# Kernel tuning notes

Measured on AMD Instinct MI355X. Metric: run time of the kernel, lower is better.

Reference implementation:

```python
import jax, jax.numpy as jnp
import numpy as np

B, T, D_IN, D_STATE, N_NEURONS, D_OUT = 256, 512, 128, 128, 2048, 64


def setup_inputs() -> dict:
    key = jax.random.key(0)
    ks = jax.random.split(key, 6)
    d_aug = D_IN + D_STATE
    seq = jax.random.normal(ks[0], (B, T, D_IN), dtype=jnp.float32)
    # hypersphere-style encoders: unit-norm rows over the augmented input space
    enc = jax.random.normal(ks[1], (N_NEURONS, d_aug), dtype=jnp.float32)
    encoders = enc / jnp.linalg.norm(enc, axis=1, keepdims=True)
    gain = jax.random.uniform(ks[2], (N_NEURONS,), minval=0.5, maxval=2.0, dtype=jnp.float32)
    bias = jax.random.normal(ks[3], (N_NEURONS,), dtype=jnp.float32)
    # decoders are analytically fit in the original; use small random values so the
    # recurrent feedback path carries nontrivial signal
    state_decoders = jax.random.normal(ks[4], (N_NEURONS, D_STATE), dtype=jnp.float32) * 0.02
    decoders = jax.random.normal(ks[5], (N_NEURONS, D_OUT), dtype=jnp.float32) * 0.02
    return {"seq": seq, "encoders": encoders, "gain": gain, "bias": bias,
            "state_decoders": state_decoders, "decoders": decoders}


def reference(seq, encoders, gain, bias, state_decoders, decoders):
    # seq: (B, T, d_in); encoders: (N, d_in+d_state); state_decoders: (N, d_state)
    b = seq.shape[0]
    d_state = state_decoders.shape[1]
    n = encoders.shape[0]
    seq_t = jnp.swapaxes(seq, 0, 1)  # (T, B, d_in)

    def step(carry, u):
        s, _ = carry  # s: (B, d_state)
        x_aug = jnp.concatenate([u, s], axis=-1)          # (B, d_in+d_state)
        a = jax.nn.relu(gain * (x_aug @ encoders.T) + bias)  # (B, N)
        return (a @ state_decoders, a), None

    init = (jnp.zeros((b, d_state), seq.dtype), jnp.zeros((b, n), seq.dtype))
    (_, a_final), _ = jax.lax.scan(step, init, seq_t)
    return a_final @ decoders  # (B, d_out)
```

## Files before the change

kernel.cpp:

```cpp
#include <hip/hip_runtime.h>


constexpr int CB   = 256;
constexpr int CT   = 512;
constexpr int DIN  = 128;
constexpr int DST  = 128;
constexpr int DOUT = 64;
constexpr int DAUG = 256;

constexpr int NBG = 8;
constexpr int NNG = 16;
constexpr int BT  = 32;
constexpr int NT  = 128;

constexpr int EPAD = 264;
constexpr int APAD = 136;

using f32x4  = __attribute__((ext_vector_type(4))) float;
using bf16x8 = __attribute__((ext_vector_type(8))) short;

__device__ __forceinline__ short f2b(float x) {
  unsigned u = __builtin_bit_cast(unsigned, x);
  u += 0x7fffu + ((u >> 16) & 1u);
  return (short)(u >> 16);
}
__device__ __forceinline__ short4 f2b4(float4 v) {
  return make_short4(f2b(v.x), f2b(v.y), f2b(v.z), f2b(v.w));
}

__global__ void nef_init(float* Sbuf, unsigned int* ctrs, float* out) {
  int idx = blockIdx.x * blockDim.x + threadIdx.x;
  int stride = gridDim.x * blockDim.x;
  for (int i = idx; i < 4 * CB * DST; i += stride) Sbuf[i] = 0.f;
  for (int i = idx; i < CB * DOUT; i += stride) out[i] = 0.f;
  if (idx < 16 * 64) ctrs[idx] = 0u;
}

__global__ void __launch_bounds__(256) nef_main(
    const float* __restrict__ seq,  const float* __restrict__ enc,
    const float* __restrict__ gainp,const float* __restrict__ biasp,
    const float* __restrict__ sdec, const float* __restrict__ dec,
    float* __restrict__ out, float* __restrict__ Sbuf, unsigned int* ctrs)
{
  __shared__ short E_lds[NT][EPAD];
  __shared__ short SDT_lds[DST][APAD];
  __shared__ short X_lds[BT][EPAD];
  __shared__ short A_lds[BT][APAD];
  __shared__ float gain_lds[NT];
  __shared__ float bias_lds[NT];

  const int tid  = threadIdx.x;
  const int bg   = blockIdx.x & 7;
  const int ng   = blockIdx.x >> 3;
  const int b0   = bg * BT;
  const int n0   = ng * NT;
  const int wave = tid >> 6;
  const int lane = tid & 63;
  const int l15  = lane & 15;
  const int lhi  = lane >> 4;
  const int kbase = lhi * 8;

  for (int i = 0; i < 32; ++i) {
    int fidx = i * 256 + tid;
    int row = fidx >> 6, c4 = fidx & 63;
    const float4 v = *(const float4*)(enc + (size_t)(n0 + row) * DAUG + (c4 << 2));
    *(short4*)&E_lds[row][c4 << 2] = f2b4(v);
  }
  for (int i = 0; i < 16; ++i) {
    int fidx = i * 256 + tid;
    int n = fidx >> 5, c4 = fidx & 31;
    const float4 v = *(const float4*)(sdec + (size_t)(n0 + n) * DST + (c4 << 2));
    SDT_lds[(c4 << 2) + 0][n] = f2b(v.x);
    SDT_lds[(c4 << 2) + 1][n] = f2b(v.y);
    SDT_lds[(c4 << 2) + 2][n] = f2b(v.z);
    SDT_lds[(c4 << 2) + 3][n] = f2b(v.w);
  }
  if (tid < NT) { gain_lds[tid] = gainp[n0 + tid]; bias_lds[tid] = biasp[n0 + tid]; }

  unsigned int* ctr = ctrs + bg * 64;
  const int nsub0 = wave * 32, nsub1 = nsub0 + 16;

  float4 pu[4];
#pragma unroll
  for (int i = 0; i < 4; ++i) {
    int fidx = i * 256 + tid;
    int row = fidx >> 5, c4 = fidx & 31;
    pu[i] = *(const float4*)(seq + ((size_t)(b0 + row) * CT + 0) * DIN + (c4 << 2));
  }

  for (int t = 0; t < CT; ++t) {
    {
      float* Sz = Sbuf + ((t + 2) & 3) * (CB * DST);
      __hip_atomic_store(&Sz[b0 * DST + ng * 256 + tid], 0.f,
                         __ATOMIC_RELAXED, __HIP_MEMORY_SCOPE_AGENT);
    }
#pragma unroll
    for (int i = 0; i < 4; ++i) {
      int fidx = i * 256 + tid;
      int row = fidx >> 5, c4 = fidx & 31;
      *(short4*)&X_lds[row][c4 << 2] = f2b4(pu[i]);
    }
    if (t + 1 < CT) {
#pragma unroll
      for (int i = 0; i < 4; ++i) {
        int fidx = i * 256 + tid;
        int row = fidx >> 5, c4 = fidx & 31;
        pu[i] = *(const float4*)(seq + ((size_t)(b0 + row) * CT + (t + 1)) * DIN + (c4 << 2));
      }
    }
    if (t > 0) {
      unsigned int tgt = 16u * (unsigned)t, guard = 0;
      while (__hip_atomic_load(ctr, __ATOMIC_RELAXED, __HIP_MEMORY_SCOPE_AGENT) < tgt) {
        __builtin_amdgcn_s_sleep(1);
        if (++guard > 100000u) break;
      }
    }
    {
      const float* Sr = Sbuf + (t & 3) * (CB * DST);
#pragma unroll
      for (int i = 0; i < 2; ++i) {
        int idx8 = i * 256 + tid;
        int row = idx8 >> 4, c8 = idx8 & 15;
        const unsigned long long* p =
            (const unsigned long long*)(Sr + (size_t)(b0 + row) * DST + c8 * 8);
        short s8[8];
#pragma unroll
        for (int q = 0; q < 4; ++q) {
          unsigned long long w = __hip_atomic_load(p + q, __ATOMIC_RELAXED,
                                                   __HIP_MEMORY_SCOPE_AGENT);
          s8[2 * q]     = f2b(__builtin_bit_cast(float, (unsigned)(w & 0xffffffffu)));
          s8[2 * q + 1] = f2b(__builtin_bit_cast(float, (unsigned)(w >> 32)));
        }
        *(short4*)&X_lds[row][DIN + c8 * 8]     = make_short4(s8[0], s8[1], s8[2], s8[3]);
        *(short4*)&X_lds[row][DIN + c8 * 8 + 4] = make_short4(s8[4], s8[5], s8[6], s8[7]);
      }
    }
    __syncthreads();

    f32x4 acc00 = {0,0,0,0}, acc01 = {0,0,0,0}, acc10 = {0,0,0,0}, acc11 = {0,0,0,0};
#pragma unroll
    for (int kk = 0; kk < 8; ++kk) {
      bf16x8 a0 = *(const bf16x8*)&X_lds[l15][kk * 32 + kbase];
      bf16x8 a1 = *(const bf16x8*)&X_lds[16 + l15][kk * 32 + kbase];
      bf16x8 e0 = *(const bf16x8*)&E_lds[nsub0 + l15][kk * 32 + kbase];
      bf16x8 e1 = *(const bf16x8*)&E_lds[nsub1 + l15][kk * 32 + kbase];
      acc00 = __builtin_amdgcn_mfma_f32_16x16x32_bf16(a0, e0, acc00, 0, 0, 0);
      acc01 = __builtin_amdgcn_mfma_f32_16x16x32_bf16(a0, e1, acc01, 0, 0, 0);
      acc10 = __builtin_amdgcn_mfma_f32_16x16x32_bf16(a1, e0, acc10, 0, 0, 0);
      acc11 = __builtin_amdgcn_mfma_f32_16x16x32_bf16(a1, e1, acc11, 0, 0, 0);
    }
    {
      const int nc0 = nsub0 + l15, nc1 = nsub1 + l15;
      const float g0 = gain_lds[nc0], bi0 = bias_lds[nc0];
      const float g1 = gain_lds[nc1], bi1 = bias_lds[nc1];
#pragma unroll
      for (int j = 0; j < 4; ++j) {
        A_lds[lhi * 4 + j][nc0]      = f2b(fmaxf(g0 * acc00[j] + bi0, 0.f));
        A_lds[lhi * 4 + j][nc1]      = f2b(fmaxf(g1 * acc01[j] + bi1, 0.f));
        A_lds[16 + lhi * 4 + j][nc0] = f2b(fmaxf(g0 * acc10[j] + bi0, 0.f));
        A_lds[16 + lhi * 4 + j][nc1] = f2b(fmaxf(g1 * acc11[j] + bi1, 0.f));
      }
    }
    __syncthreads();

    if (t != CT - 1) {
      f32x4 p00 = {0,0,0,0}, p01 = {0,0,0,0}, p10 = {0,0,0,0}, p11 = {0,0,0,0};
      const int d0 = nsub0 + l15, d1 = nsub1 + l15;
#pragma unroll
      for (int kk = 0; kk < 4; ++kk) {
        bf16x8 a0 = *(const bf16x8*)&A_lds[l15][kk * 32 + kbase];
        bf16x8 a1 = *(const bf16x8*)&A_lds[16 + l15][kk * 32 + kbase];
        bf16x8 s0 = *(const bf16x8*)&SDT_lds[d0][kk * 32 + kbase];
        bf16x8 s1 = *(const bf16x8*)&SDT_lds[d1][kk * 32 + kbase];
        p00 = __builtin_amdgcn_mfma_f32_16x16x32_bf16(a0, s0, p00, 0, 0, 0);
        p01 = __builtin_amdgcn_mfma_f32_16x16x32_bf16(a0, s1, p01, 0, 0, 0);
        p10 = __builtin_amdgcn_mfma_f32_16x16x32_bf16(a1, s0, p10, 0, 0, 0);
        p11 = __builtin_amdgcn_mfma_f32_16x16x32_bf16(a1, s1, p11, 0, 0, 0);
      }
      float* Sw = Sbuf + ((t + 1) & 3) * (CB * DST);
#pragma unroll
      for (int j = 0; j < 4; ++j) {
        unsafeAtomicAdd(&Sw[(size_t)(b0 + lhi * 4 + j) * DST + d0],      p00[j]);
        unsafeAtomicAdd(&Sw[(size_t)(b0 + lhi * 4 + j) * DST + d1],      p01[j]);
        unsafeAtomicAdd(&Sw[(size_t)(b0 + 16 + lhi * 4 + j) * DST + d0], p10[j]);
        unsafeAtomicAdd(&Sw[(size_t)(b0 + 16 + lhi * 4 + j) * DST + d1], p11[j]);
      }
      __syncthreads();
      if (tid == 0) atomicAdd(ctr, 1u);
    } else {
      f32x4 o0 = {0,0,0,0}, o1 = {0,0,0,0};
      const int ocol = wave * 16 + l15;
#pragma unroll
      for (int kk = 0; kk < 4; ++kk) {
        bf16x8 a0 = *(const bf16x8*)&A_lds[l15][kk * 32 + kbase];
        bf16x8 a1 = *(const bf16x8*)&A_lds[16 + l15][kk * 32 + kbase];
        bf16x8 bfD;
#pragma unroll
        for (int j = 0; j < 8; ++j)
          bfD[j] = f2b(dec[(size_t)(n0 + kk * 32 + kbase + j) * DOUT + ocol]);
        o0 = __builtin_amdgcn_mfma_f32_16x16x32_bf16(a0, bfD, o0, 0, 0, 0);
        o1 = __builtin_amdgcn_mfma_f32_16x16x32_bf16(a1, bfD, o1, 0, 0, 0);
      }
#pragma unroll
      for (int j = 0; j < 4; ++j) {
        unsafeAtomicAdd(&out[(size_t)(b0 + lhi * 4 + j) * DOUT + ocol], o0[j]);
        unsafeAtomicAdd(&out[(size_t)(b0 + 16 + lhi * 4 + j) * DOUT + ocol], o1[j]);
      }
    }
  }
}

extern "C" void kernel_launch(void* const* d_in, const int* in_sizes, int n_in,
                              void* d_out, int out_size, void* d_ws, size_t ws_size,
                              hipStream_t stream) {
  const float* seq   = (const float*)d_in[0];
  const float* enc   = (const float*)d_in[1];
  const float* gainp = (const float*)d_in[2];
  const float* biasp = (const float*)d_in[3];
  const float* sdec  = (const float*)d_in[4];
  const float* dec   = (const float*)d_in[5];
  float* out = (float*)d_out;

  float* Sbuf = (float*)d_ws;
  unsigned int* ctrs = (unsigned int*)((char*)d_ws + (size_t)4 * CB * DST * sizeof(float));

  nef_init<<<128, 256, 0, stream>>>(Sbuf, ctrs, out);
  nef_main<<<dim3(NBG * NNG), dim3(256), 0, stream>>>(seq, enc, gainp, biasp,
                                                      sdec, dec, out, Sbuf, ctrs);
}
```

Baseline: 1.673 ms.

## Overlap input half of encoder GEMM with state wait, use packed fp16 atomics

The encoder matmul is split so the input-driven half (first 128 K columns) is computed before waiting on the cross-block state counter, hiding part of the recurrence latency. The shared state buffer becomes packed fp16 pairs, updated with global_atomic_pk_add_f16 after a lane shuffle, which halves atomic count and traffic. Each wave now signals the counter itself after s_waitcnt instead of a block barrier plus a single thread. Next-step input staging moves to the end of the step. Accumulating the state in fp16 reduces precision in the recurrent path and adds a risk of overflow or rounding error.

```diff
diff --git a/kernel.cpp b/kernel.cpp
--- a/kernel.cpp
+++ b/kernel.cpp
@@ -27,11 +27,23 @@
 __device__ __forceinline__ short4 f2b4(float4 v) {
   return make_short4(f2b(v.x), f2b(v.y), f2b(v.z), f2b(v.w));
 }
-
-__global__ void nef_init(float* Sbuf, unsigned int* ctrs, float* out) {
+__device__ __forceinline__ float h2f(unsigned short h) {
+  return (float)__builtin_bit_cast(_Float16, h);
+}
+__device__ __forceinline__ unsigned pack_h2(float lo, float hi) {
+  unsigned short l = __builtin_bit_cast(unsigned short, (_Float16)lo);
+  unsigned short h = __builtin_bit_cast(unsigned short, (_Float16)hi);
+  return (unsigned)l | ((unsigned)h << 16);
+}
+__device__ __forceinline__ void pk_add_f16(unsigned* addr, unsigned val) {
+  asm volatile("global_atomic_pk_add_f16 %0, %1, off"
+               :: "v"((unsigned long long)addr), "v"(val) : "memory");
+}
+
+__global__ void nef_init(unsigned* Sbuf, unsigned int* ctrs, float* out) {
   int idx = blockIdx.x * blockDim.x + threadIdx.x;
   int stride = gridDim.x * blockDim.x;
-  for (int i = idx; i < 4 * CB * DST; i += stride) Sbuf[i] = 0.f;
+  for (int i = idx; i < 4 * CB * 64; i += stride) Sbuf[i] = 0u;
   for (int i = idx; i < CB * DOUT; i += stride) out[i] = 0.f;
   if (idx < 16 * 64) ctrs[idx] = 0u;
 }
@@ -40,7 +52,7 @@
     const float* __restrict__ seq,  const float* __restrict__ enc,
     const float* __restrict__ gainp,const float* __restrict__ biasp,
     const float* __restrict__ sdec, const float* __restrict__ dec,
-    float* __restrict__ out, float* __restrict__ Sbuf, unsigned int* ctrs)
+    float* __restrict__ out, unsigned* __restrict__ Sbuf, unsigned int* ctrs)
 {
   __shared__ short E_lds[NT][EPAD];
   __shared__ short SDT_lds[DST][APAD];
@@ -87,59 +99,63 @@
     int row = fidx >> 5, c4 = fidx & 31;
     pu[i] = *(const float4*)(seq + ((size_t)(b0 + row) * CT + 0) * DIN + (c4 << 2));
   }
+#pragma unroll
+  for (int i = 0; i < 4; ++i) {
+    int fidx = i * 256 + tid;
+    int row = fidx >> 5, c4 = fidx & 31;
+    *(short4*)&X_lds[row][c4 << 2] = f2b4(pu[i]);
+    pu[i] = *(const float4*)(seq + ((size_t)(b0 + row) * CT + 1) * DIN + (c4 << 2));
+  }
+  __syncthreads();
 
   for (int t = 0; t < CT; ++t) {
-    {
-      float* Sz = Sbuf + ((t + 2) & 3) * (CB * DST);
-      __hip_atomic_store(&Sz[b0 * DST + ng * 256 + tid], 0.f,
+    if (tid < 128) {
+      unsigned* Sz = Sbuf + ((t + 2) & 3) * (CB * 64);
+      __hip_atomic_store(&Sz[b0 * 64 + ng * 128 + tid], 0u,
                          __ATOMIC_RELAXED, __HIP_MEMORY_SCOPE_AGENT);
     }
-#pragma unroll
-    for (int i = 0; i < 4; ++i) {
-      int fidx = i * 256 + tid;
-      int row = fidx >> 5, c4 = fidx & 31;
-      *(short4*)&X_lds[row][c4 << 2] = f2b4(pu[i]);
-    }
-    if (t + 1 < CT) {
-#pragma unroll
-      for (int i = 0; i < 4; ++i) {
-        int fidx = i * 256 + tid;
-        int row = fidx >> 5, c4 = fidx & 31;
-        pu[i] = *(const float4*)(seq + ((size_t)(b0 + row) * CT + (t + 1)) * DIN + (c4 << 2));
-      }
-    }
+
+    f32x4 acc00 = {0,0,0,0}, acc01 = {0,0,0,0}, acc10 = {0,0,0,0}, acc11 = {0,0,0,0};
+#pragma unroll
+    for (int kk = 0; kk < 4; ++kk) {
+      bf16x8 a0 = *(const bf16x8*)&X_lds[l15][kk * 32 + kbase];
+      bf16x8 a1 = *(const bf16x8*)&X_lds[16 + l15][kk * 32 + kbase];
+      bf16x8 e0 = *(const bf16x8*)&E_lds[nsub0 + l15][kk * 32 + kbase];
+      bf16x8 e1 = *(const bf16x8*)&E_lds[nsub1 + l15][kk * 32 + kbase];
+      acc00 = __builtin_amdgcn_mfma_f32_16x16x32_bf16(a0, e0, acc00, 0, 0, 0);
+      acc01 = __builtin_amdgcn_mfma_f32_16x16x32_bf16(a0, e1, acc01, 0, 0, 0);
+      acc10 = __builtin_amdgcn_mfma_f32_16x16x32_bf16(a1, e0, acc10, 0, 0, 0);
+      acc11 = __builtin_amdgcn_mfma_f32_16x16x32_bf16(a1, e1, acc11, 0, 0, 0);
+    }
+
     if (t > 0) {
-      unsigned int tgt = 16u * (unsigned)t, guard = 0;
+      unsigned int tgt = 64u * (unsigned)t, guard = 0;
       while (__hip_atomic_load(ctr, __ATOMIC_RELAXED, __HIP_MEMORY_SCOPE_AGENT) < tgt) {
         __builtin_amdgcn_s_sleep(1);
         if (++guard > 100000u) break;
       }
     }
     {
-      const float* Sr = Sbuf + (t & 3) * (CB * DST);
-#pragma unroll
-      for (int i = 0; i < 2; ++i) {
-        int idx8 = i * 256 + tid;
-        int row = idx8 >> 4, c8 = idx8 & 15;
-        const unsigned long long* p =
-            (const unsigned long long*)(Sr + (size_t)(b0 + row) * DST + c8 * 8);
-        short s8[8];
-#pragma unroll
-        for (int q = 0; q < 4; ++q) {
-          unsigned long long w = __hip_atomic_load(p + q, __ATOMIC_RELAXED,
-                                                   __HIP_MEMORY_SCOPE_AGENT);
-          s8[2 * q]     = f2b(__builtin_bit_cast(float, (unsigned)(w & 0xffffffffu)));
-          s8[2 * q + 1] = f2b(__builtin_bit_cast(float, (unsigned)(w >> 32)));
-        }
-        *(short4*)&X_lds[row][DIN + c8 * 8]     = make_short4(s8[0], s8[1], s8[2], s8[3]);
-        *(short4*)&X_lds[row][DIN + c8 * 8 + 4] = make_short4(s8[4], s8[5], s8[6], s8[7]);
+      const unsigned long long* Sr =
+          (const unsigned long long*)(Sbuf + (t & 3) * (CB * 64));
+#pragma unroll
+      for (int i = 0; i < 4; ++i) {
+        int idx4 = i * 256 + tid;
+        int row = idx4 >> 5, c = idx4 & 31;
+        unsigned long long w = __hip_atomic_load(&Sr[(size_t)(b0 + row) * 32 + c],
+                                                 __ATOMIC_RELAXED,
+                                                 __HIP_MEMORY_SCOPE_AGENT);
+        *(short4*)&X_lds[row][DIN + c * 4] = make_short4(
+            f2b(h2f((unsigned short)(w       & 0xffffu))),
+            f2b(h2f((unsigned short)((w>>16) & 0xffffu))),
+            f2b(h2f((unsigned short)((w>>32) & 0xffffu))),
+            f2b(h2f((unsigned short)((w>>48) & 0xffffu))));
       }
     }
     __syncthreads();
 
-    f32x4 acc00 = {0,0,0,0}, acc01 = {0,0,0,0}, acc10 = {0,0,0,0}, acc11 = {0,0,0,0};
-#pragma unroll
-    for (int kk = 0; kk < 8; ++kk) {
+#pragma unroll
+    for (int kk = 4; kk < 8; ++kk) {
       bf16x8 a0 = *(const bf16x8*)&X_lds[l15][kk * 32 + kbase];
       bf16x8 a1 = *(const bf16x8*)&X_lds[16 + l15][kk * 32 + kbase];
       bf16x8 e0 = *(const bf16x8*)&E_lds[nsub0 + l15][kk * 32 + kbase];
@@ -177,16 +193,31 @@
         p10 = __builtin_amdgcn_mfma_f32_16x16x32_bf16(a1, s0, p10, 0, 0, 0);
         p11 = __builtin_amdgcn_mfma_f32_16x16x32_bf16(a1, s1, p11, 0, 0, 0);
       }
-      float* Sw = Sbuf + ((t + 1) & 3) * (CB * DST);
+      unsigned* Sw = Sbuf + ((t + 1) & 3) * (CB * 64);
+      const bool ev = (l15 & 1) == 0;
+      const int colA = ev ? (nsub0 + l15) : (nsub1 + l15 - 1);
 #pragma unroll
       for (int j = 0; j < 4; ++j) {
-        unsafeAtomicAdd(&Sw[(size_t)(b0 + lhi * 4 + j) * DST + d0],      p00[j]);
-        unsafeAtomicAdd(&Sw[(size_t)(b0 + lhi * 4 + j) * DST + d1],      p01[j]);
-        unsafeAtomicAdd(&Sw[(size_t)(b0 + 16 + lhi * 4 + j) * DST + d0], p10[j]);
-        unsafeAtomicAdd(&Sw[(size_t)(b0 + 16 + lhi * 4 + j) * DST + d1], p11[j]);
+        float x0 = __shfl_xor(p00[j], 1), x1 = __shfl_xor(p01[j], 1);
+        float lo = ev ? p00[j] : x1, hi = ev ? x0 : p01[j];
+        pk_add_f16(&Sw[(size_t)(b0 + lhi * 4 + j) * 64 + (colA >> 1)],
+                   pack_h2(lo, hi));
+        float y0 = __shfl_xor(p10[j], 1), y1 = __shfl_xor(p11[j], 1);
+        lo = ev ? p10[j] : y1; hi = ev ? y0 : p11[j];
+        pk_add_f16(&Sw[(size_t)(b0 + 16 + lhi * 4 + j) * 64 + (colA >> 1)],
+                   pack_h2(lo, hi));
+      }
+      asm volatile("s_waitcnt vmcnt(0)" ::: "memory");
+      if (lane == 0) atomicAdd(ctr, 1u);
+#pragma unroll
+      for (int i = 0; i < 4; ++i) {
+        int fidx = i * 256 + tid;
+        int row = fidx >> 5, c4 = fidx & 31;
+        *(short4*)&X_lds[row][c4 << 2] = f2b4(pu[i]);
+        if (t + 2 < CT)
+          pu[i] = *(const float4*)(seq + ((size_t)(b0 + row) * CT + (t + 2)) * DIN + (c4 << 2));
       }
       __syncthreads();
-      if (tid == 0) atomicAdd(ctr, 1u);
     } else {
       f32x4 o0 = {0,0,0,0}, o1 = {0,0,0,0};
       const int ocol = wave * 16 + l15;
@@ -221,8 +252,8 @@
   const float* dec   = (const float*)d_in[5];
   float* out = (float*)d_out;
 
-  float* Sbuf = (float*)d_ws;
-  unsigned int* ctrs = (unsigned int*)((char*)d_ws + (size_t)4 * CB * DST * sizeof(float));
+  unsigned* Sbuf = (unsigned*)d_ws;
+  unsigned int* ctrs = (unsigned int*)((char*)d_ws + (size_t)4 * CB * 64 * sizeof(unsigned));
 
   nef_init<<<128, 256, 0, stream>>>(Sbuf, ctrs, out);
   nef_main<<<dim3(NBG * NNG), dim3(256), 0, stream>>>(seq, enc, gainp, biasp,
```

Measured after the change: 2.147 ms. 28.3% more time.

## Split each block's batch tile into two independent chains to overlap recurrence latency

Applied to the files above, without the earlier changes.

Each workgroup now handles two independent 16-row batch groups, each with its own sync counter, and alternates between them within a timestep. The aim is that while one group waits for the cross-block state reduction of the other, its own compute can proceed, hiding the atomic/spin latency of the recurrence. The trade-off is half-size MFMA tiles, more __syncthreads per step, and more spin-wait points, which could add overhead. Grid size stays at 128 blocks.

```diff
diff --git a/kernel.cpp b/kernel.cpp
--- a/kernel.cpp
+++ b/kernel.cpp
@@ -8,9 +8,9 @@
 constexpr int DOUT = 64;
 constexpr int DAUG = 256;
 
-constexpr int NBG = 8;
+constexpr int NBG = 16;
 constexpr int NNG = 16;
-constexpr int BT  = 32;
+constexpr int BT  = 16;
 constexpr int NT  = 128;
 
 constexpr int EPAD = 264;
@@ -33,7 +33,7 @@
   int stride = gridDim.x * blockDim.x;
   for (int i = idx; i < 4 * CB * DST; i += stride) Sbuf[i] = 0.f;
   for (int i = idx; i < CB * DOUT; i += stride) out[i] = 0.f;
-  if (idx < 16 * 64) ctrs[idx] = 0u;
+  if (idx < NBG * 64) ctrs[idx] = 0u;
 }
 
 __global__ void __launch_bounds__(256) nef_main(
@@ -44,15 +44,16 @@
 {
   __shared__ short E_lds[NT][EPAD];
   __shared__ short SDT_lds[DST][APAD];
-  __shared__ short X_lds[BT][EPAD];
-  __shared__ short A_lds[BT][APAD];
+  __shared__ short X_lds[2][BT][EPAD];
+  __shared__ short A_lds[2][BT][APAD];
   __shared__ float gain_lds[NT];
   __shared__ float bias_lds[NT];
 
   const int tid  = threadIdx.x;
-  const int bg   = blockIdx.x & 7;
+  const int kslot= blockIdx.x & 7;
   const int ng   = blockIdx.x >> 3;
-  const int b0   = bg * BT;
+  const int bgA  = 2 * kslot,      bgB = 2 * kslot + 1;
+  const int b0A  = bgA * BT,       b0B = bgB * BT;
   const int n0   = ng * NT;
   const int wave = tid >> 6;
   const int lane = tid & 63;
@@ -77,52 +78,55 @@
   }
   if (tid < NT) { gain_lds[tid] = gainp[n0 + tid]; bias_lds[tid] = biasp[n0 + tid]; }
 
-  unsigned int* ctr = ctrs + bg * 64;
+  unsigned int* ctrA = ctrs + bgA * 64;
+  unsigned int* ctrB = ctrs + bgB * 64;
   const int nsub0 = wave * 32, nsub1 = nsub0 + 16;
 
-  float4 pu[4];
-#pragma unroll
-  for (int i = 0; i < 4; ++i) {
+  float4 puA[2], puB[2];
+#pragma unroll
+  for (int i = 0; i < 2; ++i) {
     int fidx = i * 256 + tid;
     int row = fidx >> 5, c4 = fidx & 31;
-    pu[i] = *(const float4*)(seq + ((size_t)(b0 + row) * CT + 0) * DIN + (c4 << 2));
-  }
+    puA[i] = *(const float4*)(seq + ((size_t)(b0A + row) * CT + 0) * DIN + (c4 << 2));
+    puB[i] = *(const float4*)(seq + ((size_t)(b0B + row) * CT + 0) * DIN + (c4 << 2));
+  }
+#pragma unroll
+  for (int i = 0; i < 2; ++i) {
+    int fidx = i * 256 + tid;
+    int row = fidx >> 5, c4 = fidx & 31;
+    *(short4*)&X_lds[0][row][c4 << 2] = f2b4(puA[i]);
+    *(short4*)&X_lds[1][row][c4 << 2] = f2b4(puB[i]);
+    puA[i] = *(const float4*)(seq + ((size_t)(b0A + row) * CT + 1) * DIN + (c4 << 2));
+    puB[i] = *(const float4*)(seq + ((size_t)(b0B + row) * CT + 1) * DIN + (c4 << 2));
+  }
+  __syncthreads();
 
   for (int t = 0; t < CT; ++t) {
     {
       float* Sz = Sbuf + ((t + 2) & 3) * (CB * DST);
-      __hip_atomic_store(&Sz[b0 * DST + ng * 256 + tid], 0.f,
+      int c = tid >> 7;
+      int b0c = c ? b0B : b0A;
+      __hip_atomic_store(&Sz[(size_t)b0c * DST + ng * 128 + (tid & 127)], 0.f,
                          __ATOMIC_RELAXED, __HIP_MEMORY_SCOPE_AGENT);
     }
-#pragma unroll
-    for (int i = 0; i < 4; ++i) {
-      int fidx = i * 256 + tid;
-      int row = fidx >> 5, c4 = fidx & 31;
-      *(short4*)&X_lds[row][c4 << 2] = f2b4(pu[i]);
-    }
-    if (t + 1 < CT) {
-#pragma unroll
-      for (int i = 0; i < 4; ++i) {
-        int fidx = i * 256 + tid;
-        int row = fidx >> 5, c4 = fidx & 31;
-        pu[i] = *(const float4*)(seq + ((size_t)(b0 + row) * CT + (t + 1)) * DIN + (c4 << 2));
-      }
-    }
-    if (t > 0) {
-      unsigned int tgt = 16u * (unsigned)t, guard = 0;
-      while (__hip_atomic_load(ctr, __ATOMIC_RELAXED, __HIP_MEMORY_SCOPE_AGENT) < tgt) {
-        __builtin_amdgcn_s_sleep(1);
-        if (++guard > 100000u) break;
-      }
-    }
-    {
-      const float* Sr = Sbuf + (t & 3) * (CB * DST);
-#pragma unroll
-      for (int i = 0; i < 2; ++i) {
-        int idx8 = i * 256 + tid;
-        int row = idx8 >> 4, c8 = idx8 & 15;
+
+#pragma unroll
+    for (int c = 0; c < 2; ++c) {
+      const int b0c = c ? b0B : b0A;
+      unsigned int* ctr = c ? ctrB : ctrA;
+
+      if (t > 0) {
+        unsigned int tgt = 16u * (unsigned)t, guard = 0;
+        while (__hip_atomic_load(ctr, __ATOMIC_RELAXED, __HIP_MEMORY_SCOPE_AGENT) < tgt) {
+          __builtin_amdgcn_s_sleep(1);
+          if (++guard > 100000u) break;
+        }
+      }
+      {
+        const float* Sr = Sbuf + (t & 3) * (CB * DST);
+        int row = tid >> 4, c8 = tid & 15;
         const unsigned long long* p =
-            (const unsigned long long*)(Sr + (size_t)(b0 + row) * DST + c8 * 8);
+            (const unsigned long long*)(Sr + (size_t)(b0c + row) * DST + c8 * 8);
         short s8[8];
 #pragma unroll
         for (int q = 0; q < 4; ++q) {
@@ -131,80 +135,76 @@
           s8[2 * q]     = f2b(__builtin_bit_cast(float, (unsigned)(w & 0xffffffffu)));
           s8[2 * q + 1] = f2b(__builtin_bit_cast(float, (unsigned)(w >> 32)));
         }
-        *(short4*)&X_lds[row][DIN + c8 * 8]     = make_short4(s8[0], s8[1], s8[2], s8[3]);
-        *(short4*)&X_lds[row][DIN + c8 * 8 + 4] = make_short4(s8[4], s8[5], s8[6], s8[7]);
-      }
-    }
-    __syncthreads();
-
-    f32x4 acc00 = {0,0,0,0}, acc01 = {0,0,0,0}, acc10 = {0,0,0,0}, acc11 = {0,0,0,0};
-#pragma unroll
-    for (int kk = 0; kk < 8; ++kk) {
-      bf16x8 a0 = *(const bf16x8*)&X_lds[l15][kk * 32 + kbase];
-      bf16x8 a1 = *(const bf16x8*)&X_lds[16 + l15][kk * 32 + kbase];
-      bf16x8 e0 = *(const bf16x8*)&E_lds[nsub0 + l15][kk * 32 + kbase];
-      bf16x8 e1 = *(const bf16x8*)&E_lds[nsub1 + l15][kk * 32 + kbase];
-      acc00 = __builtin_amdgcn_mfma_f32_16x16x32_bf16(a0, e0, acc00, 0, 0, 0);
-      acc01 = __builtin_amdgcn_mfma_f32_16x16x32_bf16(a0, e1, acc01, 0, 0, 0);
-      acc10 = __builtin_amdgcn_mfma_f32_16x16x32_bf16(a1, e0, acc10, 0, 0, 0);
-      acc11 = __builtin_amdgcn_mfma_f32_16x16x32_bf16(a1, e1, acc11, 0, 0, 0);
-    }
-    {
-      const int nc0 = nsub0 + l15, nc1 = nsub1 + l15;
-      const float g0 = gain_lds[nc0], bi0 = bias_lds[nc0];
-      const float g1 = gain_lds[nc1], bi1 = bias_lds[nc1];
-#pragma unroll
-      for (int j = 0; j < 4; ++j) {
-        A_lds[lhi * 4 + j][nc0]      = f2b(fmaxf(g0 * acc00[j] + bi0, 0.f));
-        A_lds[lhi * 4 + j][nc1]      = f2b(fmaxf(g1 * acc01[j] + bi1, 0.f));
-        A_lds[16 + lhi * 4 + j][nc0] = f2b(fmaxf(g0 * acc10[j] + bi0, 0.f));
-        A_lds[16 + lhi * 4 + j][nc1] = f2b(fmaxf(g1 * acc11[j] + bi1, 0.f));
-      }
-    }
-    __syncthreads();
-
-    if (t != CT - 1) {
-      f32x4 p00 = {0,0,0,0}, p01 = {0,0,0,0}, p10 = {0,0,0,0}, p11 = {0,0,0,0};
-      const int d0 = nsub0 + l15, d1 = nsub1 + l15;
-#pragma unroll
-      for (int kk = 0; kk < 4; ++kk) {
-        bf16x8 a0 = *(const bf16x8*)&A_lds[l15][kk * 32 + kbase];
-        bf16x8 a1 = *(const bf16x8*)&A_lds[16 + l15][kk * 32 + kbase];
-        bf16x8 s0 = *(const bf16x8*)&SDT_lds[d0][kk * 32 + kbase];
-        bf16x8 s1 = *(const bf16x8*)&SDT_lds[d1][kk * 32 + kbase];
-        p00 = __builtin_amdgcn_mfma_f32_16x16x32_bf16(a0, s0, p00, 0, 0, 0);
-        p01 = __builtin_amdgcn_mfma_f32_16x16x32_bf16(a0, s1, p01, 0, 0, 0);
-        p10 = __builtin_amdgcn_mfma_f32_16x16x32_bf16(a1, s0, p10, 0, 0, 0);
-        p11 = __builtin_amdgcn_mfma_f32_16x16x32_bf16(a1, s1, p11, 0, 0, 0);
-      }
-      float* Sw = Sbuf + ((t + 1) & 3) * (CB * DST);
-#pragma unroll
-      for (int j = 0; j < 4; ++j) {
-        unsafeAtomicAdd(&Sw[(size_t)(b0 + lhi * 4 + j) * DST + d0],      p00[j]);
-        unsafeAtomicAdd(&Sw[(size_t)(b0 + lhi * 4 + j) * DST + d1],      p01[j]);
-        unsafeAtomicAdd(&Sw[(size_t)(b0 + 16 + lhi * 4 + j) * DST + d0], p10[j]);
-        unsafeAtomicAdd(&Sw[(size_t)(b0 + 16 + lhi * 4 + j) * DST + d1], p11[j]);
+        *(short4*)&X_lds[c][row][DIN + c8 * 8]     = make_short4(s8[0], s8[1], s8[2], s8[3]);
+        *(short4*)&X_lds[c][row][DIN + c8 * 8 + 4] = make_short4(s8[4], s8[5], s8[6], s8[7]);
       }
       __syncthreads();
-      if (tid == 0) atomicAdd(ctr, 1u);
-    } else {
-      f32x4 o0 = {0,0,0,0}, o1 = {0,0,0,0};
-      const int ocol = wave * 16 + l15;
-#pragma unroll
-      for (int kk = 0; kk < 4; ++kk) {
-        bf16x8 a0 = *(const bf16x8*)&A_lds[l15][kk * 32 + kbase];
-        bf16x8 a1 = *(const bf16x8*)&A_lds[16 + l15][kk * 32 + kbase];
-        bf16x8 bfD;
-#pragma unroll
-        for (int j = 0; j < 8; ++j)
-          bfD[j] = f2b(dec[(size_t)(n0 + kk * 32 + kbase + j) * DOUT + ocol]);
-        o0 = __builtin_amdgcn_mfma_f32_16x16x32_bf16(a0, bfD, o0, 0, 0, 0);
-        o1 = __builtin_amdgcn_mfma_f32_16x16x32_bf16(a1, bfD, o1, 0, 0, 0);
-      }
-#pragma unroll
-      for (int j = 0; j < 4; ++j) {
-        unsafeAtomicAdd(&out[(size_t)(b0 + lhi * 4 + j) * DOUT + ocol], o0[j]);
-        unsafeAtomicAdd(&out[(size_t)(b0 + 16 + lhi * 4 + j) * DOUT + ocol], o1[j]);
+
+      f32x4 acc0 = {0,0,0,0}, acc1 = {0,0,0,0};
+#pragma unroll
+      for (int kk = 0; kk < 8; ++kk) {
+        bf16x8 a0 = *(const bf16x8*)&X_lds[c][l15][kk * 32 + kbase];
+        bf16x8 e0 = *(const bf16x8*)&E_lds[nsub0 + l15][kk * 32 + kbase];
+        bf16x8 e1 = *(const bf16x8*)&E_lds[nsub1 + l15][kk * 32 + kbase];
+        acc0 = __builtin_amdgcn_mfma_f32_16x16x32_bf16(a0, e0, acc0, 0, 0, 0);
+        acc1 = __builtin_amdgcn_mfma_f32_16x16x32_bf16(a0, e1, acc1, 0, 0, 0);
+      }
+      {
+        const int nc0 = nsub0 + l15, nc1 = nsub1 + l15;
+        const float g0 = gain_lds[nc0], bi0 = bias_lds[nc0];
+        const float g1 = gain_lds[nc1], bi1 = bias_lds[nc1];
+#pragma unroll
+        for (int j = 0; j < 4; ++j) {
+          A_lds[c][lhi * 4 + j][nc0] = f2b(fmaxf(g0 * acc0[j] + bi0, 0.f));
+          A_lds[c][lhi * 4 + j][nc1] = f2b(fmaxf(g1 * acc1[j] + bi1, 0.f));
+        }
+      }
+      __syncthreads();
+
+      if (t != CT - 1) {
+        f32x4 p0 = {0,0,0,0}, p1 = {0,0,0,0};
+        const int d0 = nsub0 + l15, d1 = nsub1 + l15;
+#pragma unroll
+        for (int kk = 0; kk < 4; ++kk) {
+          bf16x8 a0 = *(const bf16x8*)&A_lds[c][l15][kk * 32 + kbase];
+          bf16x8 s0 = *(const bf16x8*)&SDT_lds[d0][kk * 32 + kbase];
+          bf16x8 s1 = *(const bf16x8*)&SDT_lds[d1][kk * 32 + kbase];
+          p0 = __builtin_amdgcn_mfma_f32_16x16x32_bf16(a0, s0, p0, 0, 0, 0);
+          p1 = __builtin_amdgcn_mfma_f32_16x16x32_bf16(a0, s1, p1, 0, 0, 0);
+        }
+        float* Sw = Sbuf + ((t + 1) & 3) * (CB * DST);
+#pragma unroll
+        for (int j = 0; j < 4; ++j) {
+          unsafeAtomicAdd(&Sw[(size_t)(b0c + lhi * 4 + j) * DST + d0], p0[j]);
+          unsafeAtomicAdd(&Sw[(size_t)(b0c + lhi * 4 + j) * DST + d1], p1[j]);
+        }
+#pragma unroll
+        for (int i = 0; i < 2; ++i) {
+          int fidx = i * 256 + tid;
+          int row = fidx >> 5, c4 = fidx & 31;
+          float4* pu = c ? puB : puA;
+          *(short4*)&X_lds[c][row][c4 << 2] = f2b4(pu[i]);
+          if (t + 2 < CT)
+            pu[i] = *(const float4*)(seq + ((size_t)(b0c + row) * CT + (t + 2)) * DIN + (c4 << 2));
+        }
+        __syncthreads();
+        if (tid == 0) atomicAdd(ctr, 1u);
+      } else {
+        f32x4 o0 = {0,0,0,0};
+        const int ocol = wave * 16 + l15;
+#pragma unroll
+        for (int kk = 0; kk < 4; ++kk) {
+          bf16x8 a0 = *(const bf16x8*)&A_lds[c][l15][kk * 32 + kbase];
+          bf16x8 bfD;
+#pragma unroll
+          for (int j = 0; j < 8; ++j)
+            bfD[j] = f2b(dec[(size_t)(n0 + kk * 32 + kbase + j) * DOUT + ocol]);
+          o0 = __builtin_amdgcn_mfma_f32_16x16x32_bf16(a0, bfD, o0, 0, 0, 0);
+        }
+#pragma unroll
+        for (int j = 0; j < 4; ++j)
+          unsafeAtomicAdd(&out[(size_t)(b0c + lhi * 4 + j) * DOUT + ocol], o0[j]);
+        __syncthreads();
       }
     }
   }
@@ -225,6 +225,6 @@
   unsigned int* ctrs = (unsigned int*)((char*)d_ws + (size_t)4 * CB * DST * sizeof(float));
 
   nef_init<<<128, 256, 0, stream>>>(Sbuf, ctrs, out);
-  nef_main<<<dim3(NBG * NNG), dim3(256), 0, stream>>>(seq, enc, gainp, biasp,
-                                                      sdec, dec, out, Sbuf, ctrs);
-}
+  nef_main<<<dim3(8 * NNG), dim3(256), 0, stream>>>(seq, enc, gainp, biasp,
+                                                    sdec, dec, out, Sbuf, ctrs);
+}
```

Result: slower. 2.098 ms (+25.4%).

## Overlap input-half encoder GEMM with recurrent barrier; retile and keep state decoders in registers

Applied to the files above, without the earlier changes.

Each block now covers 16 batch rows and 256 neurons instead of 32 and 128, so the per-step barrier waits for 8 neuron-group blocks rather than 16. The input-half of the encoder MFMA (the first 128 K columns) is computed before spinning on the step counter, taking that work off the serial recurrent critical path. The next step's input is staged into shared memory after the state write, and seq prefetch runs two steps ahead. State decoders move from shared memory into per-wave bf16 registers, which raises register pressure. The kernel also contains some no-op gain/bias shared-memory writes.

```diff
diff --git a/kernel.cpp b/kernel.cpp
--- a/kernel.cpp
+++ b/kernel.cpp
@@ -8,13 +8,13 @@
 constexpr int DOUT = 64;
 constexpr int DAUG = 256;
 
-constexpr int NBG = 8;
-constexpr int NNG = 16;
-constexpr int BT  = 32;
-constexpr int NT  = 128;
+constexpr int NBG = 16;
+constexpr int NNG = 8;
+constexpr int BT  = 16;
+constexpr int NT  = 256;
 
 constexpr int EPAD = 264;
-constexpr int APAD = 136;
+constexpr int APAD = 264;
 
 using f32x4  = __attribute__((ext_vector_type(4))) float;
 using bf16x8 = __attribute__((ext_vector_type(8))) short;
@@ -43,15 +43,14 @@
     float* __restrict__ out, float* __restrict__ Sbuf, unsigned int* ctrs)
 {
   __shared__ short E_lds[NT][EPAD];
-  __shared__ short SDT_lds[DST][APAD];
   __shared__ short X_lds[BT][EPAD];
   __shared__ short A_lds[BT][APAD];
   __shared__ float gain_lds[NT];
   __shared__ float bias_lds[NT];
 
   const int tid  = threadIdx.x;
-  const int bg   = blockIdx.x & 7;
-  const int ng   = blockIdx.x >> 3;
+  const int bg   = blockIdx.x & 15;
+  const int ng   = blockIdx.x >> 4;
   const int b0   = bg * BT;
   const int n0   = ng * NT;
   const int wave = tid >> 6;
@@ -60,33 +59,48 @@
   const int lhi  = lane >> 4;
   const int kbase = lhi * 8;
 
-  for (int i = 0; i < 32; ++i) {
+  for (int i = 0; i < 64; ++i) {
     int fidx = i * 256 + tid;
     int row = fidx >> 6, c4 = fidx & 63;
     const float4 v = *(const float4*)(enc + (size_t)(n0 + row) * DAUG + (c4 << 2));
     *(short4*)&E_lds[row][c4 << 2] = f2b4(v);
   }
-  for (int i = 0; i < 16; ++i) {
-    int fidx = i * 256 + tid;
-    int n = fidx >> 5, c4 = fidx & 31;
-    const float4 v = *(const float4*)(sdec + (size_t)(n0 + n) * DST + (c4 << 2));
-    SDT_lds[(c4 << 2) + 0][n] = f2b(v.x);
-    SDT_lds[(c4 << 2) + 1][n] = f2b(v.y);
-    SDT_lds[(c4 << 2) + 2][n] = f2b(v.z);
-    SDT_lds[(c4 << 2) + 3][n] = f2b(v.w);
-  }
   if (tid < NT) { gain_lds[tid] = gainp[n0 + tid]; bias_lds[tid] = biasp[n0 + tid]; }
+  else if (tid < 2 * NT) {  }
+  if (tid >= NT) { gain_lds[tid & 255] = gain_lds[tid & 255]; }
+
+  bf16x8 sdt0[8], sdt1[8];
+#pragma unroll
+  for (int kk = 0; kk < 8; ++kk) {
+    bf16x8 f0, f1;
+    const int dA = wave * 32 + l15, dB = dA + 16;
+#pragma unroll
+    for (int j = 0; j < 8; ++j) {
+      const size_t nrow = (size_t)(n0 + kk * 32 + kbase + j) * DST;
+      f0[j] = f2b(sdec[nrow + dA]);
+      f1[j] = f2b(sdec[nrow + dB]);
+    }
+    sdt0[kk] = f0; sdt1[kk] = f1;
+  }
 
   unsigned int* ctr = ctrs + bg * 64;
-  const int nsub0 = wave * 32, nsub1 = nsub0 + 16;
-
-  float4 pu[4];
-#pragma unroll
-  for (int i = 0; i < 4; ++i) {
+  const int nsub = wave * 64;
+
+  float4 pu[2];
+#pragma unroll
+  for (int i = 0; i < 2; ++i) {
     int fidx = i * 256 + tid;
     int row = fidx >> 5, c4 = fidx & 31;
     pu[i] = *(const float4*)(seq + ((size_t)(b0 + row) * CT + 0) * DIN + (c4 << 2));
   }
+#pragma unroll
+  for (int i = 0; i < 2; ++i) {
+    int fidx = i * 256 + tid;
+    int row = fidx >> 5, c4 = fidx & 31;
+    *(short4*)&X_lds[row][c4 << 2] = f2b4(pu[i]);
+    pu[i] = *(const float4*)(seq + ((size_t)(b0 + row) * CT + 1) * DIN + (c4 << 2));
+  }
+  __syncthreads();
 
   for (int t = 0; t < CT; ++t) {
     {
@@ -94,22 +108,23 @@
       __hip_atomic_store(&Sz[b0 * DST + ng * 256 + tid], 0.f,
                          __ATOMIC_RELAXED, __HIP_MEMORY_SCOPE_AGENT);
     }
-#pragma unroll
-    for (int i = 0; i < 4; ++i) {
-      int fidx = i * 256 + tid;
-      int row = fidx >> 5, c4 = fidx & 31;
-      *(short4*)&X_lds[row][c4 << 2] = f2b4(pu[i]);
-    }
-    if (t + 1 < CT) {
-#pragma unroll
-      for (int i = 0; i < 4; ++i) {
-        int fidx = i * 256 + tid;
-        int row = fidx >> 5, c4 = fidx & 31;
-        pu[i] = *(const float4*)(seq + ((size_t)(b0 + row) * CT + (t + 1)) * DIN + (c4 << 2));
-      }
-    }
+
+    f32x4 acc0 = {0,0,0,0}, acc1 = {0,0,0,0}, acc2 = {0,0,0,0}, acc3 = {0,0,0,0};
+#pragma unroll
+    for (int kk = 0; kk < 4; ++kk) {
+      bf16x8 a = *(const bf16x8*)&X_lds[l15][kk * 32 + kbase];
+      bf16x8 e0 = *(const bf16x8*)&E_lds[nsub +      l15][kk * 32 + kbase];
+      bf16x8 e1 = *(const bf16x8*)&E_lds[nsub + 16 + l15][kk * 32 + kbase];
+      bf16x8 e2 = *(const bf16x8*)&E_lds[nsub + 32 + l15][kk * 32 + kbase];
+      bf16x8 e3 = *(const bf16x8*)&E_lds[nsub + 48 + l15][kk * 32 + kbase];
+      acc0 = __builtin_amdgcn_mfma_f32_16x16x32_bf16(a, e0, acc0, 0, 0, 0);
+      acc1 = __builtin_amdgcn_mfma_f32_16x16x32_bf16(a, e1, acc1, 0, 0, 0);
+      acc2 = __builtin_amdgcn_mfma_f32_16x16x32_bf16(a, e2, acc2, 0, 0, 0);
+      acc3 = __builtin_amdgcn_mfma_f32_16x16x32_bf16(a, e3, acc3, 0, 0, 0);
+    }
+
     if (t > 0) {
-      unsigned int tgt = 16u * (unsigned)t, guard = 0;
+      unsigned int tgt = 8u * (unsigned)t, guard = 0;
       while (__hip_atomic_load(ctr, __ATOMIC_RELAXED, __HIP_MEMORY_SCOPE_AGENT) < tgt) {
         __builtin_amdgcn_s_sleep(1);
         if (++guard > 100000u) break;
@@ -117,95 +132,96 @@
     }
     {
       const float* Sr = Sbuf + (t & 3) * (CB * DST);
-#pragma unroll
-      for (int i = 0; i < 2; ++i) {
-        int idx8 = i * 256 + tid;
-        int row = idx8 >> 4, c8 = idx8 & 15;
-        const unsigned long long* p =
-            (const unsigned long long*)(Sr + (size_t)(b0 + row) * DST + c8 * 8);
-        short s8[8];
-#pragma unroll
-        for (int q = 0; q < 4; ++q) {
-          unsigned long long w = __hip_atomic_load(p + q, __ATOMIC_RELAXED,
-                                                   __HIP_MEMORY_SCOPE_AGENT);
-          s8[2 * q]     = f2b(__builtin_bit_cast(float, (unsigned)(w & 0xffffffffu)));
-          s8[2 * q + 1] = f2b(__builtin_bit_cast(float, (unsigned)(w >> 32)));
-        }
-        *(short4*)&X_lds[row][DIN + c8 * 8]     = make_short4(s8[0], s8[1], s8[2], s8[3]);
-        *(short4*)&X_lds[row][DIN + c8 * 8 + 4] = make_short4(s8[4], s8[5], s8[6], s8[7]);
-      }
+      int row = tid >> 4, c8 = tid & 15;
+      const unsigned long long* p =
+          (const unsigned long long*)(Sr + (size_t)(b0 + row) * DST + c8 * 8);
+      short s8[8];
+#pragma unroll
+      for (int q = 0; q < 4; ++q) {
+        unsigned long long w = __hip_atomic_load(p + q, __ATOMIC_RELAXED,
+                                                 __HIP_MEMORY_SCOPE_AGENT);
+        s8[2 * q]     = f2b(__builtin_bit_cast(float, (unsigned)(w & 0xffffffffu)));
+        s8[2 * q + 1] = f2b(__builtin_bit_cast(float, (unsigned)(w >> 32)));
+      }
+      *(short4*)&X_lds[row][DIN + c8 * 8]     = make_short4(s8[0], s8[1], s8[2], s8[3]);
+      *(short4*)&X_lds[row][DIN + c8 * 8 + 4] = make_short4(s8[4], s8[5], s8[6], s8[7]);
     }
     __syncthreads();
 
-    f32x4 acc00 = {0,0,0,0}, acc01 = {0,0,0,0}, acc10 = {0,0,0,0}, acc11 = {0,0,0,0};
-#pragma unroll
-    for (int kk = 0; kk < 8; ++kk) {
-      bf16x8 a0 = *(const bf16x8*)&X_lds[l15][kk * 32 + kbase];
-      bf16x8 a1 = *(const bf16x8*)&X_lds[16 + l15][kk * 32 + kbase];
-      bf16x8 e0 = *(const bf16x8*)&E_lds[nsub0 + l15][kk * 32 + kbase];
-      bf16x8 e1 = *(const bf16x8*)&E_lds[nsub1 + l15][kk * 32 + kbase];
-      acc00 = __builtin_amdgcn_mfma_f32_16x16x32_bf16(a0, e0, acc00, 0, 0, 0);
-      acc01 = __builtin_amdgcn_mfma_f32_16x16x32_bf16(a0, e1, acc01, 0, 0, 0);
-      acc10 = __builtin_amdgcn_mfma_f32_16x16x32_bf16(a1, e0, acc10, 0, 0, 0);
-      acc11 = __builtin_amdgcn_mfma_f32_16x16x32_bf16(a1, e1, acc11, 0, 0, 0);
+#pragma unroll
+    for (int kk = 4; kk < 8; ++kk) {
+      bf16x8 a = *(const bf16x8*)&X_lds[l15][kk * 32 + kbase];
+      bf16x8 e0 = *(const bf16x8*)&E_lds[nsub +      l15][kk * 32 + kbase];
+      bf16x8 e1 = *(const bf16x8*)&E_lds[nsub + 16 + l15][kk * 32 + kbase];
+      bf16x8 e2 = *(const bf16x8*)&E_lds[nsub + 32 + l15][kk * 32 + kbase];
+      bf16x8 e3 = *(const bf16x8*)&E_lds[nsub + 48 + l15][kk * 32 + kbase];
+      acc0 = __builtin_amdgcn_mfma_f32_16x16x32_bf16(a, e0, acc0, 0, 0, 0);
+      acc1 = __builtin_amdgcn_mfma_f32_16x16x32_bf16(a, e1, acc1, 0, 0, 0);
+      acc2 = __builtin_amdgcn_mfma_f32_16x16x32_bf16(a, e2, acc2, 0, 0, 0);
+      acc3 = __builtin_amdgcn_mfma_f32_16x16x32_bf16(a, e3, acc3, 0, 0, 0);
     }
     {
-      const int nc0 = nsub0 + l15, nc1 = nsub1 + l15;
+      const int nc0 = nsub + l15, nc1 = nc0 + 16, nc2 = nc0 + 32, nc3 = nc0 + 48;
       const float g0 = gain_lds[nc0], bi0 = bias_lds[nc0];
       const float g1 = gain_lds[nc1], bi1 = bias_lds[nc1];
+      const float g2 = gain_lds[nc2], bi2 = bias_lds[nc2];
+      const float g3 = gain_lds[nc3], bi3 = bias_lds[nc3];
 #pragma unroll
       for (int j = 0; j < 4; ++j) {
-        A_lds[lhi * 4 + j][nc0]      = f2b(fmaxf(g0 * acc00[j] + bi0, 0.f));
-        A_lds[lhi * 4 + j][nc1]      = f2b(fmaxf(g1 * acc01[j] + bi1, 0.f));
-        A_lds[16 + lhi * 4 + j][nc0] = f2b(fmaxf(g0 * acc10[j] + bi0, 0.f));
-        A_lds[16 + lhi * 4 + j][nc1] = f2b(fmaxf(g1 * acc11[j] + bi1, 0.f));
+        A_lds[lhi * 4 + j][nc0] = f2b(fmaxf(g0 * acc0[j] + bi0, 0.f));
+        A_lds[lhi * 4 + j][nc1] = f2b(fmaxf(g1 * acc1[j] + bi1, 0.f));
+        A_lds[lhi * 4 + j][nc2] = f2b(fmaxf(g2 * acc2[j] + bi2, 0.f));
+        A_lds[lhi * 4 + j][nc3] = f2b(fmaxf(g3 * acc3[j] + bi3, 0.f));
       }
     }
     __syncthreads();
 
     if (t != CT - 1) {
-      f32x4 p00 = {0,0,0,0}, p01 = {0,0,0,0}, p10 = {0,0,0,0}, p11 = {0,0,0,0};
-      const int d0 = nsub0 + l15, d1 = nsub1 + l15;
-#pragma unroll
-      for (int kk = 0; kk < 4; ++kk) {
-        bf16x8 a0 = *(const bf16x8*)&A_lds[l15][kk * 32 + kbase];
-        bf16x8 a1 = *(const bf16x8*)&A_lds[16 + l15][kk * 32 + kbase];
-        bf16x8 s0 = *(const bf16x8*)&SDT_lds[d0][kk * 32 + kbase];
-        bf16x8 s1 = *(const bf16x8*)&SDT_lds[d1][kk * 32 + kbase];
-        p00 = __builtin_amdgcn_mfma_f32_16x16x32_bf16(a0, s0, p00, 0, 0, 0);
-        p01 = __builtin_amdgcn_mfma_f32_16x16x32_bf16(a0, s1, p01, 0, 0, 0);
-        p10 = __builtin_amdgcn_mfma_f32_16x16x32_bf16(a1, s0, p10, 0, 0, 0);
-        p11 = __builtin_amdgcn_mfma_f32_16x16x32_bf16(a1, s1, p11, 0, 0, 0);
+      f32x4 p0 = {0,0,0,0}, p1 = {0,0,0,0};
+#pragma unroll
+      for (int kk = 0; kk < 8; ++kk) {
+        bf16x8 a = *(const bf16x8*)&A_lds[l15][kk * 32 + kbase];
+        p0 = __builtin_amdgcn_mfma_f32_16x16x32_bf16(a, sdt0[kk], p0, 0, 0, 0);
+        p1 = __builtin_amdgcn_mfma_f32_16x16x32_bf16(a, sdt1[kk], p1, 0, 0, 0);
       }
       float* Sw = Sbuf + ((t + 1) & 3) * (CB * DST);
+      const int dA = wave * 32 + l15, dB = dA + 16;
 #pragma unroll
       for (int j = 0; j < 4; ++j) {
-        unsafeAtomicAdd(&Sw[(size_t)(b0 + lhi * 4 + j) * DST + d0],      p00[j]);
-        unsafeAtomicAdd(&Sw[(size_t)(b0 + lhi * 4 + j) * DST + d1],      p01[j]);
-        unsafeAtomicAdd(&Sw[(size_t)(b0 + 16 + lhi * 4 + j) * DST + d0], p10[j]);
-        unsafeAtomicAdd(&Sw[(size_t)(b0 + 16 + lhi * 4 + j) * DST + d1], p11[j]);
+        unsafeAtomicAdd(&Sw[(size_t)(b0 + lhi * 4 + j) * DST + dA], p0[j]);
+        unsafeAtomicAdd(&Sw[(size_t)(b0 + lhi * 4 + j) * DST + dB], p1[j]);
+      }
+#pragma unroll
+      for (int i = 0; i < 2; ++i) {
+        int fidx = i * 256 + tid;
+        int row = fidx >> 5, c4 = fidx & 31;
+        *(short4*)&X_lds[row][c4 << 2] = f2b4(pu[i]);
       }
       __syncthreads();
       if (tid == 0) atomicAdd(ctr, 1u);
+      if (t + 2 < CT) {
+#pragma unroll
+        for (int i = 0; i < 2; ++i) {
+          int fidx = i * 256 + tid;
+          int row = fidx >> 5, c4 = fidx & 31;
+          pu[i] = *(const float4*)(seq + ((size_t)(b0 + row) * CT + (t + 2)) * DIN + (c4 << 2));
+        }
+      }
     } else {
-      f32x4 o0 = {0,0,0,0}, o1 = {0,0,0,0};
+      f32x4 o0 = {0,0,0,0};
       const int ocol = wave * 16 + l15;
 #pragma unroll
-      for (int kk = 0; kk < 4; ++kk) {
-        bf16x8 a0 = *(const bf16x8*)&A_lds[l15][kk * 32 + kbase];
-        bf16x8 a1 = *(const bf16x8*)&A_lds[16 + l15][kk * 32 + kbase];
+      for (int kk = 0; kk < 8; ++kk) {
+        bf16x8 a = *(const bf16x8*)&A_lds[l15][kk * 32 + kbase];
         bf16x8 bfD;
 #pragma unroll
         for (int j = 0; j < 8; ++j)
           bfD[j] = f2b(dec[(size_t)(n0 + kk * 32 + kbase + j) * DOUT + ocol]);
-        o0 = __builtin_amdgcn_mfma_f32_16x16x32_bf16(a0, bfD, o0, 0, 0, 0);
-        o1 = __builtin_amdgcn_mfma_f32_16x16x32_bf16(a1, bfD, o1, 0, 0, 0);
-      }
-#pragma unroll
-      for (int j = 0; j < 4; ++j) {
+        o0 = __builtin_amdgcn_mfma_f32_16x16x32_bf16(a, bfD, o0, 0, 0, 0);
+      }
+#pragma unroll
+      for (int j = 0; j < 4; ++j)
         unsafeAtomicAdd(&out[(size_t)(b0 + lhi * 4 + j) * DOUT + ocol], o0[j]);
-        unsafeAtomicAdd(&out[(size_t)(b0 + 16 + lhi * 4 + j) * DOUT + ocol], o1[j]);
-      }
     }
   }
 }
```

Measured after the change: 1.505 ms. 10.0% less time.
